# Kernel optimization log

Hardware: AMD Instinct MI355X
Metric: run time of the kernel (lower is better)

The kernel has to match this reference:

```python
import jax, jax.numpy as jnp
import numpy as np

N = 50000   # nodes
E = 1600000 # edges
D = 128     # feature dim (in = hidden = 128)


def setup_inputs() -> dict:
    key = jax.random.key(0)
    k1, k2, k3, k4 = jax.random.split(key, 4)
    scale = 1.0 / np.sqrt(D)
    return {
        "x": jax.random.normal(k1, (N, D), jnp.float32),
        "edge_index": jax.random.randint(k2, (2, E), 0, N, dtype=jnp.int32),
        "W0": jax.random.normal(k3, (D, D), jnp.float32) * scale,
        "b0": jnp.zeros((D,), jnp.float32),
        "W1": jax.random.normal(k4, (D, D), jnp.float32) * scale,
        "b1": jnp.zeros((D,), jnp.float32),
    }


def _gcn_norm(edge_index, num_nodes):
    # Add self-loops, compute symmetric normalization D^-1/2 A_hat D^-1/2.
    loop = jnp.arange(num_nodes, dtype=edge_index.dtype)
    src = jnp.concatenate([edge_index[0], loop])
    dst = jnp.concatenate([edge_index[1], loop])
    deg = jax.ops.segment_sum(jnp.ones_like(dst, jnp.float32), dst,
                              num_segments=num_nodes)
    dinv = jnp.where(deg > 0, jax.lax.rsqrt(deg), 0.0)
    norm = dinv[dst] * dinv[src]  # [E+N]
    return src, dst, norm


def _gcn_layer(x, src, dst, norm, W, b, num_nodes):
    h = x @ W                                  # [N, D]
    msg = h[src] * norm[:, None]               # gather + scale  [E+N, D]
    out = jax.ops.segment_sum(msg, dst, num_segments=num_nodes)  # scatter-add
    return out + b


def reference(x, edge_index, W0, b0, W1, b1):
    num_nodes = x.shape[0]
    src, dst, norm = _gcn_norm(edge_index, num_nodes)
    # forward loops over the first k=2 convs, ReLU after each (as in source)
    x = jax.nn.relu(_gcn_layer(x, src, dst, norm, W0, b0, num_nodes))
    x = jax.nn.relu(_gcn_layer(x, src, dst, norm, W1, b1, num_nodes))
    return x
```

## Files before the change

### kernel.cpp

```cpp
#include <hip/hip_runtime.h>
#include <hip/hip_bf16.h>

#define D 128
#define CHUNK 8192
#define SPAN_CAP 768


typedef __attribute__((ext_vector_type(8))) short short8;
typedef __attribute__((ext_vector_type(4))) float floatx4;

static __device__ inline unsigned int f2bf(float f) {
    unsigned int u = __float_as_uint(f);
    return (u + 0x7FFFu + ((u >> 16) & 1u)) >> 16;
}
static __device__ inline float bflo(unsigned int u) { return __uint_as_float(u << 16); }
static __device__ inline float bfhi(unsigned int u) { return __uint_as_float(u & 0xFFFF0000u); }

__global__ __launch_bounds__(256) void k01_swz_hist(const float* __restrict__ W0,
                                                    const float* __restrict__ W1,
                                                    short8* __restrict__ whi0, short8* __restrict__ wlo0,
                                                    short8* __restrict__ whi1, short8* __restrict__ wlo1,
                                                    const int* __restrict__ dst,
                                                    int* __restrict__ blockhist, int E_) {
    __shared__ int h[256];
    const int tid = threadIdx.x;
    if (blockIdx.x < 16) {
        int gid = blockIdx.x * 256 + tid;
        const float* W = (gid < 2048) ? W0 : W1;
        short8* whi = (gid < 2048) ? whi0 : whi1;
        short8* wlo = (gid < 2048) ? wlo0 : wlo1;
        int t2 = gid & 2047;
        int t = t2 >> 8, q = (t2 >> 6) & 3, lane = t2 & 63;
        short8 hi, lo;
        #pragma unroll
        for (int j = 0; j < 8; ++j) {
            int k = q * 32 + (lane >> 4) * 8 + j;
            int n = t * 16 + (lane & 15);
            float w = W[k * D + n];
            unsigned int hh = f2bf(w);
            hi[j] = (short)hh;
            lo[j] = (short)f2bf(w - __uint_as_float(hh << 16));
        }
        whi[t2] = hi;
        wlo[t2] = lo;
    } else {
        const int b = blockIdx.x - 16;
        h[tid] = 0;
        __syncthreads();
        const int e0 = b * CHUNK;
        const int e1 = min(E_, e0 + CHUNK);
        for (int e = e0 + tid; e < e1; e += 256)
            atomicAdd(&h[dst[e] >> 8], 1);
        __syncthreads();
        blockhist[b * 256 + tid] = h[tid];
    }
}

__global__ __launch_bounds__(256) void k23_scan_scatter(const int* __restrict__ blockhist,
                                                        const int* __restrict__ dst,
                                                        const int* __restrict__ src,
                                                        int* __restrict__ bucket_offs,
                                                        unsigned int* __restrict__ buf,
                                                        int NB, int NBUK, int E_) {
    __shared__ int s[256];
    __shared__ int c[256];
    const int myb = blockIdx.x, tid = threadIdx.x;
    int total = 0, prefix = 0;
    #pragma unroll 4
    for (int b2 = 0; b2 < NB; ++b2) {
        int t = blockhist[b2 * 256 + tid];
        total += t;
        prefix += (b2 < myb) ? t : 0;
    }
    s[tid] = total;
    __syncthreads();
    #pragma unroll
    for (int off = 1; off < 256; off <<= 1) {
        int x = (tid >= off) ? s[tid - off] : 0;
        __syncthreads();
        s[tid] += x;
        __syncthreads();
    }
    int bstart = s[tid] - total;
    if (myb == 0) {
        if (tid < NBUK) bucket_offs[tid] = bstart;
        if (tid == 0) bucket_offs[NBUK] = E_;
    }
    c[tid] = bstart + prefix;
    __syncthreads();

    const int e0 = myb * CHUNK;
    const int e1 = min(E_, e0 + CHUNK);
    for (int e = e0 + tid; e < e1; e += 256) {
        int v = dst[e];
        int sdx = src[e];
        int pos = atomicAdd(&c[v >> 8], 1);
        buf[pos] = (unsigned int)sdx | ((unsigned int)(v & 255) << 16);
    }
}

__global__ __launch_bounds__(256) void k4_bucket(const unsigned int* __restrict__ buf,
                                                 const int* __restrict__ bucket_offs,
                                                 int* __restrict__ offs,
                                                 float* __restrict__ dinv,
                                                 int* __restrict__ col, int N_, int E_) {
    __shared__ int h[256];
    __shared__ int s[256];
    __shared__ int c[256];
    const int beta = blockIdx.x, tid = threadIdx.x;
    const int start = bucket_offs[beta];
    const int end   = bucket_offs[beta + 1];

    h[tid] = 0;
    __syncthreads();
    for (int e = start + tid; e < end; e += 256)
        atomicAdd(&h[(buf[e] >> 16) & 255], 1);
    __syncthreads();

    int deg = h[tid];
    s[tid] = deg;
    __syncthreads();
    #pragma unroll
    for (int off = 1; off < 256; off <<= 1) {
        int x = (tid >= off) ? s[tid - off] : 0;
        __syncthreads();
        s[tid] += x;
        __syncthreads();
    }
    int excl = s[tid] - deg;

    int v0 = beta * 256 + tid;
    if (v0 < N_) {
        offs[v0] = start + excl;
        dinv[v0] = rsqrtf((float)(deg + 1));
    }
    if (beta == 0 && tid == 0) offs[N_] = E_;
    c[tid] = start + excl;
    __syncthreads();

    for (int e = start + tid; e < end; e += 256) {
        unsigned int p = buf[e];
        int pos = atomicAdd(&c[(p >> 16) & 255], 1);
        col[pos] = (int)(p & 0xFFFFu);
    }
}

__global__ __launch_bounds__(256) void gemm_mfma(const float* __restrict__ A,
                                                 const short8* __restrict__ whi,
                                                 const short8* __restrict__ wlo,
                                                 const float* __restrict__ dinv,
                                                 unsigned int* __restrict__ Gu, int nrows) {
    __shared__ float tileT[128][65];

    const int tid  = threadIdx.x;
    const int wave = tid >> 6, lane = tid & 63;
    const int m = lane & 15, quad = lane >> 4;
    const int rowInBlk = wave * 16;
    const int arow = min(blockIdx.x * 64 + rowInBlk + m, nrows - 1);
    const float* Ap = A + (size_t)arow * D + quad * 8;

    floatx4 acc[8];
    #pragma unroll
    for (int t = 0; t < 8; ++t) acc[t] = (floatx4){0.f, 0.f, 0.f, 0.f};

    #pragma unroll
    for (int q = 0; q < 4; ++q) {
        float4 a0 = *(const float4*)(Ap + q * 32);
        float4 a1 = *(const float4*)(Ap + q * 32 + 4);
        float av[8] = {a0.x, a0.y, a0.z, a0.w, a1.x, a1.y, a1.z, a1.w};
        short8 ahi, alo;
        #pragma unroll
        for (int j = 0; j < 8; ++j) {
            unsigned int h = f2bf(av[j]);
            ahi[j] = (short)h;
            alo[j] = (short)f2bf(av[j] - __uint_as_float(h << 16));
        }
        #pragma unroll
        for (int t = 0; t < 8; ++t) {
            short8 bh = whi[(t * 4 + q) * 64 + lane];
            short8 bl = wlo[(t * 4 + q) * 64 + lane];
            acc[t] = __builtin_amdgcn_mfma_f32_16x16x32_bf16(ahi, bh, acc[t], 0, 0, 0);
            acc[t] = __builtin_amdgcn_mfma_f32_16x16x32_bf16(alo, bh, acc[t], 0, 0, 0);
            acc[t] = __builtin_amdgcn_mfma_f32_16x16x32_bf16(ahi, bl, acc[t], 0, 0, 0);
        }
    }

    #pragma unroll
    for (int t = 0; t < 8; ++t)
        #pragma unroll
        for (int r = 0; r < 4; ++r)
            tileT[t * 16 + m][rowInBlk + quad * 4 + r] = acc[t][r];
    __syncthreads();

    const int orow = tid >> 2, seg = tid & 3;
    const int grow = blockIdx.x * 64 + orow;
    if (grow < nrows) {
        float s = dinv[grow];
        unsigned int* Gp = Gu + (size_t)grow * 64 + seg * 16;
        #pragma unroll
        for (int i = 0; i < 4; ++i) {
            int c0 = seg * 32 + i * 8;
            uint4 o4;
            o4.x = f2bf(tileT[c0 + 0][orow] * s) | (f2bf(tileT[c0 + 1][orow] * s) << 16);
            o4.y = f2bf(tileT[c0 + 2][orow] * s) | (f2bf(tileT[c0 + 3][orow] * s) << 16);
            o4.z = f2bf(tileT[c0 + 4][orow] * s) | (f2bf(tileT[c0 + 5][orow] * s) << 16);
            o4.w = f2bf(tileT[c0 + 6][orow] * s) | (f2bf(tileT[c0 + 7][orow] * s) << 16);
            ((uint4*)Gp)[i] = o4;
        }
    }
}

__global__ __launch_bounds__(256) void aggregate_kernel(const unsigned int* __restrict__ Gu,
                                                        const int* __restrict__ offs,
                                                        const int* __restrict__ col,
                                                        const float* __restrict__ dinv,
                                                        const float* __restrict__ bias,
                                                        float* __restrict__ out, int nnodes) {
    __shared__ int scol[SPAN_CAP];
    __shared__ int soffs[9];
    const int tid   = threadIdx.x;
    const int node0 = blockIdx.x * 8;

    if (tid < 9) soffs[tid] = offs[min(node0 + tid, nnodes)];
    __syncthreads();
    const int s0   = soffs[0];
    const int span = soffs[8] - s0;
    const bool lds_ok = (span <= SPAN_CAP);
    if (lds_ok) {
        for (int k = tid; k < span; k += 256) scol[k] = col[s0 + k];
    }
    __syncthreads();

    const int lane = tid & 31;
    const int node = node0 + (tid >> 5);
    if (node >= nnodes) return;

    const unsigned int* Pl = Gu + 2 * lane;
    #define LDROW(j) (*(const uint2*)(Pl + (size_t)(j) * 64))

    uint2 su = LDROW(node);
    float a0 = bflo(su.x), a1 = bfhi(su.x), a2 = bflo(su.y), a3 = bfhi(su.y);

    const int s = soffs[tid >> 5];
    const int e = soffs[(tid >> 5) + 1];

    if (lds_ok) {
        const int b0  = s - s0;
        const int deg = e - s;
        int k = 0;
        for (; k + 8 <= deg; k += 8) {
            int j0 = scol[b0 + k + 0], j1 = scol[b0 + k + 1], j2 = scol[b0 + k + 2], j3 = scol[b0 + k + 3];
            int j4 = scol[b0 + k + 4], j5 = scol[b0 + k + 5], j6 = scol[b0 + k + 6], j7 = scol[b0 + k + 7];
            uint2 u0 = LDROW(j0);
            uint2 u1 = LDROW(j1);
            uint2 u2 = LDROW(j2);
            uint2 u3 = LDROW(j3);
            uint2 u4 = LDROW(j4);
            uint2 u5 = LDROW(j5);
            uint2 u6 = LDROW(j6);
            uint2 u7 = LDROW(j7);
            a0 += ((bflo(u0.x) + bflo(u1.x)) + (bflo(u2.x) + bflo(u3.x))) +
                  ((bflo(u4.x) + bflo(u5.x)) + (bflo(u6.x) + bflo(u7.x)));
            a1 += ((bfhi(u0.x) + bfhi(u1.x)) + (bfhi(u2.x) + bfhi(u3.x))) +
                  ((bfhi(u4.x) + bfhi(u5.x)) + (bfhi(u6.x) + bfhi(u7.x)));
            a2 += ((bflo(u0.y) + bflo(u1.y)) + (bflo(u2.y) + bflo(u3.y))) +
                  ((bflo(u4.y) + bflo(u5.y)) + (bflo(u6.y) + bflo(u7.y)));
            a3 += ((bfhi(u0.y) + bfhi(u1.y)) + (bfhi(u2.y) + bfhi(u3.y))) +
                  ((bfhi(u4.y) + bfhi(u5.y)) + (bfhi(u6.y) + bfhi(u7.y)));
        }
        for (; k + 4 <= deg; k += 4) {
            int j0 = scol[b0 + k + 0], j1 = scol[b0 + k + 1], j2 = scol[b0 + k + 2], j3 = scol[b0 + k + 3];
            uint2 u0 = LDROW(j0);
            uint2 u1 = LDROW(j1);
            uint2 u2 = LDROW(j2);
            uint2 u3 = LDROW(j3);
            a0 += (bflo(u0.x) + bflo(u1.x)) + (bflo(u2.x) + bflo(u3.x));
            a1 += (bfhi(u0.x) + bfhi(u1.x)) + (bfhi(u2.x) + bfhi(u3.x));
            a2 += (bflo(u0.y) + bflo(u1.y)) + (bflo(u2.y) + bflo(u3.y));
            a3 += (bfhi(u0.y) + bfhi(u1.y)) + (bfhi(u2.y) + bfhi(u3.y));
        }
        for (; k < deg; ++k) {
            uint2 u = LDROW(scol[b0 + k]);
            a0 += bflo(u.x);
            a1 += bfhi(u.x);
            a2 += bflo(u.y);
            a3 += bfhi(u.y);
        }
    } else {
        int idx = s;
        for (; idx + 4 <= e; idx += 4) {
            int j0 = col[idx + 0], j1 = col[idx + 1], j2 = col[idx + 2], j3 = col[idx + 3];
            uint2 u0 = LDROW(j0);
            uint2 u1 = LDROW(j1);
            uint2 u2 = LDROW(j2);
            uint2 u3 = LDROW(j3);
            a0 += (bflo(u0.x) + bflo(u1.x)) + (bflo(u2.x) + bflo(u3.x));
            a1 += (bfhi(u0.x) + bfhi(u1.x)) + (bfhi(u2.x) + bfhi(u3.x));
            a2 += (bflo(u0.y) + bflo(u1.y)) + (bflo(u2.y) + bflo(u3.y));
            a3 += (bfhi(u0.y) + bfhi(u1.y)) + (bfhi(u2.y) + bfhi(u3.y));
        }
        for (; idx < e; ++idx) {
            uint2 u = LDROW(col[idx]);
            a0 += bflo(u.x);
            a1 += bfhi(u.x);
            a2 += bflo(u.y);
            a3 += bfhi(u.y);
        }
    }
    #undef LDROW

    float dv = dinv[node];
    float4 bb = ((const float4*)bias)[lane];
    float4 o;
    o.x = fmaxf(fmaf(dv, a0, bb.x), 0.f);
    o.y = fmaxf(fmaf(dv, a1, bb.y), 0.f);
    o.z = fmaxf(fmaf(dv, a2, bb.z), 0.f);
    o.w = fmaxf(fmaf(dv, a3, bb.w), 0.f);
    ((float4*)out)[(size_t)node * 32 + lane] = o;
}

extern "C" void kernel_launch(void* const* d_in, const int* in_sizes, int n_in,
                              void* d_out, int out_size, void* d_ws, size_t ws_size,
                              hipStream_t stream) {
    const float* x    = (const float*)d_in[0];
    const int*   edge = (const int*)d_in[1];
    const float* W0   = (const float*)d_in[2];
    const float* b0   = (const float*)d_in[3];
    const float* W1   = (const float*)d_in[4];
    const float* b1   = (const float*)d_in[5];
    float* out = (float*)d_out;

    const int N_ = in_sizes[0] / D;
    const int E_ = in_sizes[1] / 2;
    const int* srcp = edge;
    const int* dstp = edge + E_;

    const int NB   = (E_ + CHUNK - 1) / CHUNK;
    const int NBUK = (N_ + 255) >> 8;

    char* p = (char*)d_ws;
    auto carve = [&](size_t bytes) { char* q = p; p += (bytes + 255) & ~(size_t)255; return q; };
    int*          blockhist = (int*)          carve((size_t)NB * 256 * 4);
    int*          buck_offs = (int*)          carve((size_t)(NBUK + 1) * 4);
    int*          offs      = (int*)          carve((size_t)(N_ + 1) * 4);
    float*        dinv      = (float*)        carve((size_t)N_ * 4);
    unsigned int* buf       = (unsigned int*) carve((size_t)E_ * 4);
    int*          col       = (int*)          carve((size_t)E_ * 4);
    unsigned int* gu        = (unsigned int*) carve((size_t)N_ * 64 * 4);
    short8*       whi0      = (short8*)       carve(2048 * 16);
    short8*       wlo0      = (short8*)       carve(2048 * 16);
    short8*       whi1      = (short8*)       carve(2048 * 16);
    short8*       wlo1      = (short8*)       carve(2048 * 16);

    k01_swz_hist   <<<16 + NB, 256, 0, stream>>>(W0, W1, whi0, wlo0, whi1, wlo1,
                                                 dstp, blockhist, E_);
    k23_scan_scatter<<<NB,     256, 0, stream>>>(blockhist, dstp, srcp, buck_offs, buf,
                                                 NB, NBUK, E_);
    k4_bucket      <<<NBUK,    256, 0, stream>>>(buf, buck_offs, offs, dinv, col, N_, E_);

    const int gmb     = (N_ + 63) / 64;
    const int ngroups = (N_ + 7) / 8;

    gemm_mfma       <<<gmb,     256, 0, stream>>>(x, whi0, wlo0, dinv, gu, N_);
    aggregate_kernel<<<ngroups, 256, 0, stream>>>(gu, offs, col, dinv, b0, out, N_);
    gemm_mfma       <<<gmb,     256, 0, stream>>>(out, whi1, wlo1, dinv, gu, N_);
    aggregate_kernel<<<ngroups, 256, 0, stream>>>(gu, offs, col, dinv, b1, out, N_);
}
```

Before: 268.7 us.

## Split gathered features into XCD-affine column planes for aggregation

The bf16 GEMM output is stored as four column planes of 32 features each, so every plane is an N×64-byte array. The aggregation blocks are remapped so each pair of XCDs handles one plane, with 8 lanes per node and 32 nodes per block. The goal is for each XCD's L2 to hold only a quarter of the gathered feature table, which should raise cache hit rates for the random neighbor gathers. The trade-off is that each edge's column index is now read four times, and there are more blocks. The change also adds nontemporal loads and stores and raises the LDS span cap to match the larger node groups.

```diff
diff --git a/kernel.cpp b/kernel.cpp
--- a/kernel.cpp
+++ b/kernel.cpp
@@ -3,7 +3,7 @@
 
 #define D 128
 #define CHUNK 8192
-#define SPAN_CAP 768
+#define SPAN_CAP 1280
 
 
 typedef __attribute__((ext_vector_type(8))) short short8;
@@ -196,7 +196,7 @@
     const int grow = blockIdx.x * 64 + orow;
     if (grow < nrows) {
         float s = dinv[grow];
-        unsigned int* Gp = Gu + (size_t)grow * 64 + seg * 16;
+        unsigned int* Gp = Gu + ((size_t)seg * nrows + grow) * 16;
         #pragma unroll
         for (int i = 0; i < 4; ++i) {
             int c0 = seg * 32 + i * 8;
@@ -215,34 +215,41 @@
                                                         const int* __restrict__ col,
                                                         const float* __restrict__ dinv,
                                                         const float* __restrict__ bias,
-                                                        float* __restrict__ out, int nnodes) {
+                                                        float* __restrict__ out, int nnodes,
+                                                        int ngroups) {
     __shared__ int scol[SPAN_CAP];
-    __shared__ int soffs[9];
+    __shared__ int soffs[33];
+    const int bid   = blockIdx.x;
+    const int xcd   = bid & 7;
+    const int plane = xcd >> 1;
+    const int i     = (bid >> 3) * 2 + (xcd & 1);
+    if (i >= ngroups) return;
     const int tid   = threadIdx.x;
-    const int node0 = blockIdx.x * 8;
-
-    if (tid < 9) soffs[tid] = offs[min(node0 + tid, nnodes)];
+    const int node0 = i * 32;
+
+    if (tid < 33) soffs[tid] = offs[min(node0 + tid, nnodes)];
     __syncthreads();
     const int s0   = soffs[0];
-    const int span = soffs[8] - s0;
+    const int span = soffs[32] - s0;
     const bool lds_ok = (span <= SPAN_CAP);
     if (lds_ok) {
-        for (int k = tid; k < span; k += 256) scol[k] = col[s0 + k];
-    }
-    __syncthreads();
-
-    const int lane = tid & 31;
-    const int node = node0 + (tid >> 5);
+        for (int k = tid; k < span; k += 256)
+            scol[k] = __builtin_nontemporal_load(&col[s0 + k]);
+    }
+    __syncthreads();
+
+    const int lane = tid & 7;
+    const int node = node0 + (tid >> 3);
     if (node >= nnodes) return;
 
-    const unsigned int* Pl = Gu + 2 * lane;
-    #define LDROW(j) (*(const uint2*)(Pl + (size_t)(j) * 64))
+    const unsigned int* Pl = Gu + (size_t)plane * nnodes * 16 + 2 * lane;
+    #define LDROW(j) (*(const uint2*)(Pl + (size_t)(j) * 16))
 
     uint2 su = LDROW(node);
     float a0 = bflo(su.x), a1 = bfhi(su.x), a2 = bflo(su.y), a3 = bfhi(su.y);
 
-    const int s = soffs[tid >> 5];
-    const int e = soffs[(tid >> 5) + 1];
+    const int s = soffs[tid >> 3];
+    const int e = soffs[(tid >> 3) + 1];
 
     if (lds_ok) {
         const int b0  = s - s0;
@@ -310,13 +317,13 @@
     #undef LDROW
 
     float dv = dinv[node];
-    float4 bb = ((const float4*)bias)[lane];
-    float4 o;
-    o.x = fmaxf(fmaf(dv, a0, bb.x), 0.f);
-    o.y = fmaxf(fmaf(dv, a1, bb.y), 0.f);
-    o.z = fmaxf(fmaf(dv, a2, bb.z), 0.f);
-    o.w = fmaxf(fmaf(dv, a3, bb.w), 0.f);
-    ((float4*)out)[(size_t)node * 32 + lane] = o;
+    float4 bb = ((const float4*)bias)[plane * 8 + lane];
+    floatx4 o;
+    o[0] = fmaxf(fmaf(dv, a0, bb.x), 0.f);
+    o[1] = fmaxf(fmaf(dv, a1, bb.y), 0.f);
+    o[2] = fmaxf(fmaf(dv, a2, bb.z), 0.f);
+    o[3] = fmaxf(fmaf(dv, a3, bb.w), 0.f);
+    __builtin_nontemporal_store(o, (floatx4*)out + (size_t)node * 32 + plane * 8 + lane);
 }
 
 extern "C" void kernel_launch(void* const* d_in, const int* in_sizes, int n_in,
@@ -359,10 +366,11 @@
     k4_bucket      <<<NBUK,    256, 0, stream>>>(buf, buck_offs, offs, dinv, col, N_, E_);
 
     const int gmb     = (N_ + 63) / 64;
-    const int ngroups = (N_ + 7) / 8;
-
-    gemm_mfma       <<<gmb,     256, 0, stream>>>(x, whi0, wlo0, dinv, gu, N_);
-    aggregate_kernel<<<ngroups, 256, 0, stream>>>(gu, offs, col, dinv, b0, out, N_);
-    gemm_mfma       <<<gmb,     256, 0, stream>>>(out, whi1, wlo1, dinv, gu, N_);
-    aggregate_kernel<<<ngroups, 256, 0, stream>>>(gu, offs, col, dinv, b1, out, N_);
-}
+    const int ngroups = (N_ + 31) / 32;
+    const int agrid   = ((ngroups + 1) / 2) * 8;
+
+    gemm_mfma       <<<gmb,   256, 0, stream>>>(x, whi0, wlo0, dinv, gu, N_);
+    aggregate_kernel<<<agrid, 256, 0, stream>>>(gu, offs, col, dinv, b0, out, N_, ngroups);
+    gemm_mfma       <<<gmb,   256, 0, stream>>>(out, whi1, wlo1, dinv, gu, N_);
+    aggregate_kernel<<<agrid, 256, 0, stream>>>(gu, offs, col, dinv, b1, out, N_, ngroups);
+}
```

Result: no change. 273.7 us (+1.8%).
